# Optimization experiments

Measured on AMD Instinct MI355X. Metric: run time of the kernel, lower is better.

Reference implementation:

```python
import jax, jax.numpy as jnp
import numpy as np

# Dimensions (babyGPT-50m: GPT-2-small-ish)
B, T, V, C, H, L = 2, 1024, 50257, 768, 12, 6
D = C // H
STD = 0.02
EPS = 1e-5


def _normal(k, shape):
    return (jax.random.normal(k, shape, dtype=jnp.float32) * STD)


def setup_inputs() -> dict:
    key = jax.random.key(0)
    ks = jax.random.split(key, 12)
    inp = {
        "idx": jax.random.randint(ks[0], (B, T), 0, V, dtype=jnp.int64 if jax.config.jax_enable_x64 else jnp.int32),
        "tok_emb": _normal(ks[1], (V, C)),
        "pos_emb": _normal(ks[2], (1, T, C)),
        # per-layer params stacked along leading L axis
        "ln1_g": jnp.ones((L, C), jnp.float32),
        "ln1_b": jnp.zeros((L, C), jnp.float32),
        "Wq": _normal(ks[3], (L, C, C)), "bq": jnp.zeros((L, C), jnp.float32),
        "Wk": _normal(ks[4], (L, C, C)), "bk": jnp.zeros((L, C), jnp.float32),
        "Wv": _normal(ks[5], (L, C, C)), "bv": jnp.zeros((L, C), jnp.float32),
        "Wp": _normal(ks[6], (L, C, C)), "bp": jnp.zeros((L, C), jnp.float32),
        "ln2_g": jnp.ones((L, C), jnp.float32),
        "ln2_b": jnp.zeros((L, C), jnp.float32),
        "Wf1": _normal(ks[7], (L, C, 4 * C)), "bf1": jnp.zeros((L, 4 * C), jnp.float32),
        "Wf2": _normal(ks[8], (L, 4 * C, C)), "bf2": jnp.zeros((L, C), jnp.float32),
        "lnf_g": jnp.ones((C,), jnp.float32),
        "lnf_b": jnp.zeros((C,), jnp.float32),
        "head_W": _normal(ks[9], (C, V)),  # head has bias=False
    }
    return inp


def _ln(x, g, b):
    m = jnp.mean(x, axis=-1, keepdims=True)
    v = jnp.var(x, axis=-1, keepdims=True)
    return (x - m) * jax.lax.rsqrt(v + EPS) * g + b


def _gpt_forward(idx, tok_emb, pos_emb, ln1_g, ln1_b, Wq, bq, Wk, bk, Wv, bv,
                 Wp, bp, ln2_g, ln2_b, Wf1, bf1, Wf2, bf2, lnf_g, lnf_b, head_W):
    x = tok_emb[idx] + pos_emb[:, :T]          # [B,T,C]; dropout is identity (eval)
    causal = jnp.tril(jnp.ones((T, T), bool))  # same tril mask as the buffer
    scale = 1.0 / np.sqrt(D).astype(np.float32)

    def block(x, p):
        g1, b1, wq, bq_, wk, bk_, wv, bv_, wp, bp_, g2, b2, w1, b1f, w2, b2f = p
        h = _ln(x, g1, b1)
        q = (h @ wq + bq_).reshape(B, T, H, D)
        k = (h @ wk + bk_).reshape(B, T, H, D)
        v = (h @ wv + bv_).reshape(B, T, H, D)
        att = jnp.einsum('bthd,bshd->bhts', q, k) * scale   # [B,H,T,T]
        att = jnp.where(causal, att, jnp.float32(-10000.0))  # masked_fill value
        att = jax.nn.softmax(att, axis=-1)
        y = jnp.einsum('bhts,bshd->bthd', att, v).reshape(B, T, C)
        x = x + y @ wp + bp_
        h2 = _ln(x, g2, b2)
        ff = jax.nn.gelu(h2 @ w1 + b1f, approximate=False) @ w2 + b2f  # exact GELU, dropout=eval
        return x + ff, None

    layer_params = (ln1_g, ln1_b, Wq, bq, Wk, bk, Wv, bv, Wp, bp,
                    ln2_g, ln2_b, Wf1, bf1, Wf2, bf2)
    x, _ = jax.lax.scan(block, x, layer_params)
    x = _ln(x, lnf_g, lnf_b)
    return x @ head_W  # logits [B,T,V]


def reference(idx, tok_emb, pos_emb, ln1_g, ln1_b, Wq, bq, Wk, bk, Wv, bv,
              Wp, bp, ln2_g, ln2_b, Wf1, bf1, Wf2, bf2, lnf_g, lnf_b, head_W):
    return _gpt_forward(idx, tok_emb, pos_emb, ln1_g, ln1_b, Wq, bq, Wk, bk, Wv, bv,
                        Wp, bp, ln2_g, ln2_b, Wf1, bf1, Wf2, bf2, lnf_g, lnf_b, head_W)
```

## Files before the change

### kernel.cpp

```cpp
#include <hip/hip_runtime.h>
#include <hip/hip_bf16.h>
#include <math.h>

#define Bsz 2
#define Tt 1024
#define Vv 50257
#define Cc 768
#define Hh 12
#define Ll 6
#define NTOK (Bsz*Tt)
#define VPAD 50304

typedef __attribute__((ext_vector_type(8))) short bf16x8;
typedef __attribute__((ext_vector_type(8))) unsigned short u16x8;
typedef __attribute__((ext_vector_type(4))) unsigned short u16x4;
typedef __attribute__((ext_vector_type(4))) float f32x4;
typedef unsigned short u16;

static __device__ __forceinline__ u16 f2bf(float f){
  unsigned u = __float_as_uint(f);
  u += 0x7FFF + ((u >> 16) & 1);
  return (u16)(u >> 16);
}
static __device__ __forceinline__ float bf2f(u16 h){
  return __uint_as_float(((unsigned)h) << 16);
}

#define GL16(g,l) __builtin_amdgcn_global_load_lds( \
    (const __attribute__((address_space(1))) void*)(g), \
    (__attribute__((address_space(3))) void*)(l), 16, 0, 0)
#define WAITVM(n) asm volatile("s_waitcnt vmcnt(%0)" :: "n"(n) : "memory")

__global__ void embed_kernel(const int* __restrict__ idx, const float* __restrict__ tok,
                             const float* __restrict__ pos, float* __restrict__ x){
  const int C4 = Cc/4;
  int i = blockIdx.x * 256 + threadIdx.x;
  if (i >= NTOK*C4) return;
  int tk = i / C4, c4 = i % C4;
  int row = idx[tk];
  int t = tk % Tt;
  float4 a = ((const float4*)tok)[(size_t)row*C4 + c4];
  float4 p = ((const float4*)pos)[(size_t)t*C4 + c4];
  float4 r; r.x=a.x+p.x; r.y=a.y+p.y; r.z=a.z+p.z; r.w=a.w+p.w;
  ((float4*)x)[i] = r;
}

__global__ void ln_kernel(const float* __restrict__ in, const float* __restrict__ g,
                          const float* __restrict__ bt, u16* __restrict__ out){
  int row = blockIdx.x, tid = threadIdx.x;
  const float* r = in + (size_t)row*Cc;
  float v0=r[tid], v1=r[tid+256], v2=r[tid+512];
  float s  = v0+v1+v2;
  float s2 = v0*v0+v1*v1+v2*v2;
  #pragma unroll
  for (int off=32; off; off>>=1){ s += __shfl_xor(s,off); s2 += __shfl_xor(s2,off); }
  __shared__ float red[8];
  int wid = tid >> 6;
  if ((tid & 63) == 0){ red[wid]=s; red[4+wid]=s2; }
  __syncthreads();
  float S  = red[0]+red[1]+red[2]+red[3];
  float S2 = red[4]+red[5]+red[6]+red[7];
  float mean = S * (1.0f/Cc);
  float var  = S2 * (1.0f/Cc) - mean*mean;
  float rstd = rsqrtf(var + 1e-5f);
  u16* o = out + (size_t)row*Cc;
  o[tid]     = f2bf((v0-mean)*rstd*g[tid]     + bt[tid]);
  o[tid+256] = f2bf((v1-mean)*rstd*g[tid+256] + bt[tid+256]);
  o[tid+512] = f2bf((v2-mean)*rstd*g[tid+512] + bt[tid+512]);
}

__global__ void wtrans_kernel(const float* __restrict__ in, u16* __restrict__ out,
                              int K, int N, int Npad, size_t lsi, size_t lso){
  __shared__ float t[64][33];
  const float* inp = in + (size_t)blockIdx.z*lsi;
  u16* op = out + (size_t)blockIdx.z*lso;
  int n0 = blockIdx.x*32, k0 = blockIdx.y*64;
  int tx = threadIdx.x, ty = threadIdx.y;
  #pragma unroll
  for (int i=0;i<8;i++){
    int k = k0+ty+i*8, n = n0+tx;
    t[ty+i*8][tx] = (n < N) ? inp[(size_t)k*N + n] : 0.f;
  }
  __syncthreads();
  #pragma unroll
  for (int i=0;i<2;i++){
    int nl = i*16 + ty*2 + (tx>>4);
    int kl = (tx&15)*4;
    int n = n0 + nl;
    if (n < Npad){
      u16x4 pk;
      pk[0] = f2bf(t[kl+0][nl]); pk[1] = f2bf(t[kl+1][nl]);
      pk[2] = f2bf(t[kl+2][nl]); pk[3] = f2bf(t[kl+3][nl]);
      *(u16x4*)&op[(size_t)n*K + k0 + kl] = pk;
    }
  }
}

__global__ void vtrans_kernel(const u16* __restrict__ qkv, u16* __restrict__ vT){
  __shared__ u16 s[32][33];
  int bh = blockIdx.z; int b = bh/Hh, h = bh - b*Hh;
  int t0 = blockIdx.x*32, d0 = blockIdx.y*32;
  int tx=threadIdx.x, ty=threadIdx.y;
  #pragma unroll
  for (int i=0;i<4;i++)
    s[ty+i*8][tx] = qkv[(size_t)(b*Tt + t0+ty+i*8)*2304 + 1536 + h*64 + d0 + tx];
  __syncthreads();
  #pragma unroll
  for (int i=0;i<4;i++)
    vT[((size_t)bh*64 + d0+ty+i*8)*Tt + t0 + tx] = s[tx][ty+i*8];
}

__global__ void bconcat_kernel(const float* __restrict__ bq, const float* __restrict__ bk,
                               const float* __restrict__ bv, float* __restrict__ o){
  int i = blockIdx.x*256 + threadIdx.x;
  if (i >= Ll*2304) return;
  int l = i/2304, j = i - l*2304;
  o[i] = (j < 768) ? bq[l*768+j] : (j < 1536) ? bk[l*768+j-768] : bv[l*768+j-1536];
}

__global__ __launch_bounds__(256) void flash_kernel(
    const u16* __restrict__ qkv, const u16* __restrict__ vT, u16* __restrict__ y){
  __shared__ u16 Ks[2][64*64];
  __shared__ u16 Vs[2][64*64];
  __shared__ u16 Ps[4][32*64];
  int bx = blockIdx.x;
  int bh = blockIdx.y; int b = bh/Hh, h = bh - b*Hh;
  int q0 = bx*128;
  int tid = threadIdx.x, lane = tid&63, wid = tid>>6;
  const size_t tokbase = (size_t)b*Tt;
  int arow = lane&15, akof = (lane>>4)*8;
  bf16x8 qa[2][2];
  #pragma unroll
  for (int mi=0;mi<2;mi++)
    #pragma unroll
    for (int ks=0;ks<2;ks++)
      qa[mi][ks] = *(const bf16x8*)&qkv[(tokbase + q0 + wid*32 + mi*16 + arow)*2304
                                        + h*64 + ks*32 + akof];
  int srow = lane>>3;
  int sbyte = ((lane&7)*16) ^ (srow<<4);
  const u16* kbase = qkv + tokbase*2304 + 768 + h*64;
  const u16* vbase = vT + (size_t)bh*64*Tt;
  auto STAGEKV = [&](int t, int bb){
    int j0 = t*64;
    #pragma unroll
    for (int c=0;c<2;c++){
      int r = wid*16 + c*8 + srow;
      GL16(kbase + (size_t)(j0 + r)*2304 + (sbyte>>1), &Ks[bb][(wid*16 + c*8)*64]);
      GL16(vbase + (size_t)r*Tt + j0 + (sbyte>>1),     &Vs[bb][(wid*16 + c*8)*64]);
    }
  };
  float m_r[2][4], l_r[2][4];
  f32x4 o_acc[2][4] = {};
  #pragma unroll
  for (int mi=0;mi<2;mi++)
    #pragma unroll
    for (int jj=0;jj<4;jj++){ m_r[mi][jj] = -1e30f; l_r[mi][jj] = 0.f; }

  int njt = 2*bx + 2;
  STAGEKV(0, 0);
  asm volatile("s_waitcnt vmcnt(0)" ::: "memory");
  __builtin_amdgcn_s_barrier();
  for (int t=0; t<njt; t++){
    int cur = t&1;
    if (t+1 < njt) STAGEKV(t+1, cur^1);
    int j0 = t*64;
    f32x4 sacc[2][4] = {};
    #pragma unroll
    for (int ks=0;ks<2;ks++){
      bf16x8 kf[4];
      #pragma unroll
      for (int ni=0;ni<4;ni++){
        int s16 = ni*16 + (lane&15);
        int kb = (ks*64 + (lane>>4)*16) ^ ((s16&7)<<4);
        kf[ni] = *(const bf16x8*)((const char*)&Ks[cur][0] + s16*128 + kb);
      }
      #pragma unroll
      for (int mi=0;mi<2;mi++)
        #pragma unroll
        for (int ni=0;ni<4;ni++)
          sacc[mi][ni] = __builtin_amdgcn_mfma_f32_16x16x32_bf16(qa[mi][ks], kf[ni], sacc[mi][ni], 0,0,0);
    }
    float tmax[2][4];
    #pragma unroll
    for (int mi=0;mi<2;mi++)
      #pragma unroll
      for (int jj=0;jj<4;jj++) tmax[mi][jj] = -1e30f;
    #pragma unroll
    for (int mi=0;mi<2;mi++)
      #pragma unroll
      for (int ni=0;ni<4;ni++)
        #pragma unroll
        for (int jj=0;jj<4;jj++){
          float v = sacc[mi][ni][jj]*0.125f;
          int sg = j0 + ni*16 + (lane&15);
          int tg = q0 + wid*32 + mi*16 + (lane>>4)*4 + jj;
          v = (sg <= tg) ? v : -1e30f;
          sacc[mi][ni][jj] = v;
          tmax[mi][jj] = fmaxf(tmax[mi][jj], v);
        }
    #pragma unroll
    for (int mi=0;mi<2;mi++)
      #pragma unroll
      for (int jj=0;jj<4;jj++){
        float tm = tmax[mi][jj];
        tm = fmaxf(tm, __shfl_xor(tm,1)); tm = fmaxf(tm, __shfl_xor(tm,2));
        tm = fmaxf(tm, __shfl_xor(tm,4)); tm = fmaxf(tm, __shfl_xor(tm,8));
        float mn = fmaxf(m_r[mi][jj], tm);
        float al = __expf(m_r[mi][jj] - mn);
        m_r[mi][jj] = mn;
        l_r[mi][jj] *= al;
        tmax[mi][jj] = al;
      }
    float tsum[2][4] = {};
    #pragma unroll
    for (int mi=0;mi<2;mi++)
      #pragma unroll
      for (int ni=0;ni<4;ni++)
        #pragma unroll
        for (int jj=0;jj<4;jj++){
          float p = __expf(sacc[mi][ni][jj] - m_r[mi][jj]);
          tsum[mi][jj] += p;
          int pr = mi*16 + (lane>>4)*4 + jj;
          int pcb = (2*(ni*16 + (lane&15))) ^ ((pr&7)<<4);
          *(u16*)((char*)&Ps[wid][0] + pr*128 + pcb) = f2bf(p);
        }
    #pragma unroll
    for (int mi=0;mi<2;mi++)
      #pragma unroll
      for (int jj=0;jj<4;jj++){
        float ts = tsum[mi][jj];
        ts += __shfl_xor(ts,1); ts += __shfl_xor(ts,2);
        ts += __shfl_xor(ts,4); ts += __shfl_xor(ts,8);
        l_r[mi][jj] += ts;
        float al = tmax[mi][jj];
        #pragma unroll
        for (int ni2=0;ni2<4;ni2++) o_acc[mi][ni2][jj] *= al;
      }
    #pragma unroll
    for (int ks2=0;ks2<2;ks2++){
      bf16x8 pa[2], vf[4];
      #pragma unroll
      for (int mi=0;mi<2;mi++){
        int prr = mi*16 + (lane&15);
        int pb = (ks2*64 + (lane>>4)*16) ^ ((prr&7)<<4);
        pa[mi] = *(const bf16x8*)((const char*)&Ps[wid][0] + prr*128 + pb);
      }
      #pragma unroll
      for (int ni2=0;ni2<4;ni2++){
        int d16 = ni2*16 + (lane&15);
        int sb = (ks2*64 + (lane>>4)*16) ^ ((d16&7)<<4);
        vf[ni2] = *(const bf16x8*)((const char*)&Vs[cur][0] + d16*128 + sb);
      }
      #pragma unroll
      for (int mi=0;mi<2;mi++)
        #pragma unroll
        for (int ni2=0;ni2<4;ni2++)
          o_acc[mi][ni2] = __builtin_amdgcn_mfma_f32_16x16x32_bf16(pa[mi], vf[ni2], o_acc[mi][ni2], 0,0,0);
    }
    asm volatile("s_waitcnt vmcnt(0) lgkmcnt(0)" ::: "memory");
    __builtin_amdgcn_s_barrier();
  }
  #pragma unroll
  for (int mi=0;mi<2;mi++)
    #pragma unroll
    for (int jj=0;jj<4;jj++){
      float inv = 1.0f / l_r[mi][jj];
      int tok2 = q0 + wid*32 + mi*16 + (lane>>4)*4 + jj;
      size_t rb = (tokbase + tok2)*Cc + h*64;
      #pragma unroll
      for (int ni2=0;ni2<4;ni2++)
        y[rb + ni2*16 + (lane&15)] = f2bf(o_acc[mi][ni2][jj] * inv);
    }
}

template<int BM, int BN, bool BIAS, bool RESID, bool GELU, bool OUTBF, bool ROWSCAN>
__global__ __launch_bounds__(256) void mm_kernel(
    const u16* __restrict__ A, const u16* __restrict__ Bm,
    const float* __restrict__ bias, const float* __restrict__ resid,
    void* __restrict__ out, int N, int K, int lda, int ldb, int ldc)
{
  constexpr int FM   = BM/32;
  constexpr int FN   = BN/32;
  constexpr int CPW  = FN*16;
  constexpr int ESTR = CPW + 4;
  constexpr int ABUF = BM*32;
  constexpr int BBUF = BN*32;
  constexpr int LOADS = (BM+BN)/64;
  constexpr int SMEM_STAGE = 3*(ABUF+BBUF)*2;
  constexpr int SMEM_EPI   = 4*16*ESTR*4;
  constexpr int SMEMB = SMEM_STAGE > SMEM_EPI ? SMEM_STAGE : SMEM_EPI;
  __shared__ __align__(16) char smem[SMEMB];
  u16* As = (u16*)smem;
  u16* Bs = As + 3*ABUF;

  int bx = blockIdx.x, by = blockIdx.y;
  {
    int gx = gridDim.x;
    int nwg = gx * gridDim.y;
    int flat = by*gx + bx;
    int qq = nwg >> 3, rr = nwg & 7;
    int xcd = flat & 7, lid = flat >> 3;
    int swz = (xcd < rr) ? xcd*(qq+1) + lid : rr*(qq+1) + (xcd-rr)*qq + lid;
    bx = swz % gx; by = swz / gx;
  }
  int m0 = bx*BM, n0 = by*BN;
  int tid = threadIdx.x, lane = tid & 63, wid = tid >> 6;
  int wr = wid >> 1, wc = wid & 1;
  int r0 = wr*(BM/2), c0 = wc*(BN/2);
  int lrow = lane & 15, koff = (lane >> 4)*8;
  int sr = lane >> 2, sk = (lane & 3)*8;
  const u16* Ap = A + (size_t)(m0 + wid*(BM/4) + sr)*lda + sk;
  const u16* Bp = Bm + (size_t)(n0 + wid*(BN/4) + sr)*ldb + sk;
  int nt = K/32;
  auto STAGE = [&](int t, int bb){
    int kk = t*32;
    u16* Al = As + bb*ABUF + wid*(ABUF/4);
    GL16(Ap + kk, Al);
    if constexpr (BM==128) GL16(Ap + kk + (size_t)16*lda, Al + 512);
    u16* Bl = Bs + bb*BBUF + wid*(BBUF/4);
    GL16(Bp + kk, Bl);
    if constexpr (BN==128) GL16(Bp + kk + (size_t)16*ldb, Bl + 512);
  };
  f32x4 acc[FM][FN] = {};
  STAGE(0, 0);
  if (nt > 1) STAGE(1, 1);
  WAITVM(LOADS);
  __builtin_amdgcn_s_barrier();
  for (int t = 0; t < nt; t++){
    int bb = t % 3;
    if (t+2 < nt) STAGE(t+2, (t+2)%3);
    const u16* Ab2 = As + bb*ABUF;
    const u16* Bb2 = Bs + bb*BBUF;
    bf16x8 af[FM], bfr[FN];
    #pragma unroll
    for (int m=0;m<FM;m++) af[m] = *(const bf16x8*)&Ab2[(r0 + m*16 + lrow)*32 + koff];
    #pragma unroll
    for (int n=0;n<FN;n++) bfr[n] = *(const bf16x8*)&Bb2[(c0 + n*16 + lrow)*32 + koff];
    #pragma unroll
    for (int m=0;m<FM;m++)
      #pragma unroll
      for (int n=0;n<FN;n++)
        acc[m][n] = __builtin_amdgcn_mfma_f32_16x16x32_bf16(af[m], bfr[n], acc[m][n], 0,0,0);
    if (t+2 < nt) WAITVM(LOADS); else WAITVM(0);
    __builtin_amdgcn_s_barrier();
  }

  float* ebuf = (float*)smem + wid*16*ESTR;
  int er = lane >> 2;
  int ec = (lane & 3) * (CPW/4);
  #pragma unroll
  for (int m=0;m<FM;m++){
    #pragma unroll
    for (int n=0;n<FN;n++)
      #pragma unroll
      for (int j=0;j<4;j++)
        ebuf[((lane>>4)*4+j)*ESTR + n*16 + (lane&15)] = acc[m][n][j];
    __builtin_amdgcn_s_waitcnt(0);
    if constexpr (ROWSCAN){
      #pragma unroll
      for (int rr2=0; rr2<16; rr2++){
        int gr2 = m0 + r0 + m*16 + rr2;
        int gc2 = n0 + c0 + lane;
        float v = ebuf[rr2*ESTR + lane];
        if (gc2 < N) ((float*)out)[(size_t)gr2*ldc + gc2] = v;
      }
    } else {
      int grow = m0 + r0 + m*16 + er;
      int gcol = n0 + c0 + ec;
      size_t rbase = (size_t)grow*ldc;
      if constexpr (OUTBF){
        u16 tmp[CPW/4];
        #pragma unroll
        for (int q=0;q<FN;q++){
          float4 v = *(const float4*)&ebuf[er*ESTR + ec + q*4];
          float f0=v.x, f1=v.y, f2=v.z, f3=v.w;
          if (BIAS){
            float4 b4 = *(const float4*)&bias[gcol + q*4];
            f0+=b4.x; f1+=b4.y; f2+=b4.z; f3+=b4.w;
          }
          if (GELU){
            f0 = 0.5f*f0*(1.f+erff(f0*0.70710678118654752f));
            f1 = 0.5f*f1*(1.f+erff(f1*0.70710678118654752f));
            f2 = 0.5f*f2*(1.f+erff(f2*0.70710678118654752f));
            f3 = 0.5f*f3*(1.f+erff(f3*0.70710678118654752f));
          }
          tmp[q*4+0]=f2bf(f0); tmp[q*4+1]=f2bf(f1);
          tmp[q*4+2]=f2bf(f2); tmp[q*4+3]=f2bf(f3);
        }
        #pragma unroll
        for (int s2=0; s2<CPW/32; s2++)
          *(u16x8*)&((u16*)out)[rbase + gcol + s2*8] = *(const u16x8*)&tmp[s2*8];
      } else {
        #pragma unroll
        for (int q=0;q<FN;q++){
          float4 v = *(const float4*)&ebuf[er*ESTR + ec + q*4];
          float f0=v.x, f1=v.y, f2=v.z, f3=v.w;
          if (BIAS){
            float4 b4 = *(const float4*)&bias[gcol + q*4];
            f0+=b4.x; f1+=b4.y; f2+=b4.z; f3+=b4.w;
          }
          if (GELU){
            f0 = 0.5f*f0*(1.f+erff(f0*0.70710678118654752f));
            f1 = 0.5f*f1*(1.f+erff(f1*0.70710678118654752f));
            f2 = 0.5f*f2*(1.f+erff(f2*0.70710678118654752f));
            f3 = 0.5f*f3*(1.f+erff(f3*0.70710678118654752f));
          }
          if (RESID){
            float4 r4 = *(const float4*)&resid[rbase + gcol + q*4];
            f0+=r4.x; f1+=r4.y; f2+=r4.z; f3+=r4.w;
          }
          float4 o4; o4.x=f0; o4.y=f1; o4.z=f2; o4.w=f3;
          *(float4*)&((float*)out)[rbase + gcol + q*4] = o4;
        }
      }
    }
  }
}

extern "C" void kernel_launch(void* const* d_in, const int* in_sizes, int n_in,
                              void* d_out, int out_size, void* d_ws, size_t ws_size,
                              hipStream_t stream){
  const int*   idx  = (const int*)d_in[0];
  const float* tok  = (const float*)d_in[1];
  const float* pos  = (const float*)d_in[2];
  const float* ln1g = (const float*)d_in[3];
  const float* ln1b = (const float*)d_in[4];
  const float* Wq   = (const float*)d_in[5];
  const float* bq   = (const float*)d_in[6];
  const float* Wk   = (const float*)d_in[7];
  const float* bk   = (const float*)d_in[8];
  const float* Wv   = (const float*)d_in[9];
  const float* bv   = (const float*)d_in[10];
  const float* Wp   = (const float*)d_in[11];
  const float* bp   = (const float*)d_in[12];
  const float* ln2g = (const float*)d_in[13];
  const float* ln2b = (const float*)d_in[14];
  const float* Wf1  = (const float*)d_in[15];
  const float* bf1  = (const float*)d_in[16];
  const float* Wf2  = (const float*)d_in[17];
  const float* bf2  = (const float*)d_in[18];
  const float* lnfg = (const float*)d_in[19];
  const float* lnfb = (const float*)d_in[20];
  const float* headW= (const float*)d_in[21];
  float* outp = (float*)d_out;

  char* w = (char*)d_ws;
  u16* wqkvT = (u16*)w;  w += (size_t)Ll*2304*768*2;
  u16* wpT   = (u16*)w;  w += (size_t)Ll*768*768*2;
  u16* wf1T  = (u16*)w;  w += (size_t)Ll*3072*768*2;
  u16* wf2T  = (u16*)w;  w += (size_t)Ll*768*3072*2;
  u16* headT = (u16*)w;  w += (size_t)VPAD*768*2;
  float* bqkv= (float*)w;w += (size_t)Ll*2304*4;
  float* x   = (float*)w;w += (size_t)NTOK*Cc*4;
  u16* h     = (u16*)w;  w += (size_t)NTOK*Cc*2;
  u16* qkv   = (u16*)w;  w += (size_t)NTOK*2304*2;
  u16* vT    = (u16*)w;  w += (size_t)Bsz*Hh*64*Tt*2;
  u16* y     = (u16*)w;  w += (size_t)NTOK*Cc*2;
  u16* ff    = (u16*)w;  w += (size_t)NTOK*4*Cc*2;

  dim3 tb(32,8);
  wtrans_kernel<<<dim3(24,12,Ll), tb, 0, stream>>>(Wq, wqkvT,          768, 768, 768, (size_t)Cc*Cc, (size_t)2304*768);
  wtrans_kernel<<<dim3(24,12,Ll), tb, 0, stream>>>(Wk, wqkvT+768*768,  768, 768, 768, (size_t)Cc*Cc, (size_t)2304*768);
  wtrans_kernel<<<dim3(24,12,Ll), tb, 0, stream>>>(Wv, wqkvT+1536*768, 768, 768, 768, (size_t)Cc*Cc, (size_t)2304*768);
  wtrans_kernel<<<dim3(24,12,Ll), tb, 0, stream>>>(Wp, wpT,            768, 768, 768, (size_t)Cc*Cc, (size_t)768*768);
  wtrans_kernel<<<dim3(96,12,Ll), tb, 0, stream>>>(Wf1, wf1T,          768, 3072, 3072, (size_t)Cc*4*Cc, (size_t)3072*768);
  wtrans_kernel<<<dim3(24,48,Ll), tb, 0, stream>>>(Wf2, wf2T,          3072, 768, 768, (size_t)4*Cc*Cc, (size_t)768*3072);
  wtrans_kernel<<<dim3(VPAD/32,12,1), tb, 0, stream>>>(headW, headT, 768, Vv, VPAD, 0, 0);
  bconcat_kernel<<<(Ll*2304+255)/256, 256, 0, stream>>>(bq, bk, bv, bqkv);

  embed_kernel<<<NTOK*(Cc/4)/256, 256, 0, stream>>>(idx, tok, pos, x);

  for (int l=0;l<Ll;l++){
    ln_kernel<<<NTOK, 256, 0, stream>>>(x, ln1g+l*Cc, ln1b+l*Cc, h);
    mm_kernel<64,128,true,false,false,true,false><<<dim3(32,18,1), 256, 0, stream>>>(
        h, wqkvT+(size_t)l*2304*768, bqkv+l*2304, nullptr, qkv, 2304, 768, 768, 768, 2304);
    vtrans_kernel<<<dim3(32,2,Bsz*Hh), tb, 0, stream>>>(qkv, vT);
    flash_kernel<<<dim3(Tt/128, Bsz*Hh), 256, 0, stream>>>(qkv, vT, y);
    mm_kernel<64,64,true,true,false,false,false><<<dim3(32,12,1), 256, 0, stream>>>(
        y, wpT+(size_t)l*768*768, bp+l*Cc, x, x, 768, 768, 768, 768, 768);
    ln_kernel<<<NTOK, 256, 0, stream>>>(x, ln2g+l*Cc, ln2b+l*Cc, h);
    mm_kernel<64,128,true,false,true,true,false><<<dim3(32,24,1), 256, 0, stream>>>(
        h, wf1T+(size_t)l*3072*768, bf1+(size_t)l*4*Cc, nullptr, ff, 3072, 768, 768, 768, 3072);
    mm_kernel<64,64,true,true,false,false,false><<<dim3(32,12,1), 256, 0, stream>>>(
        ff, wf2T+(size_t)l*768*3072, bf2+l*Cc, x, x, 768, 3072, 3072, 3072, 768);
  }
  ln_kernel<<<NTOK, 256, 0, stream>>>(x, lnfg, lnfb, h);
  mm_kernel<128,128,false,false,false,false,true><<<dim3(16,VPAD/128,1), 256, 0, stream>>>(
      h, headT, nullptr, nullptr, outp, Vv, 768, 768, 768, Vv);
}
```

Measured before the change: 1.330 ms.

## Shrink flash query tile, double-buffer head GEMM, nontemporal logits stores

The flash attention kernel now processes 64 query rows per block, one 16-row MFMA tile per wave, instead of 128. This doubles the grid and lowers register and LDS use, which should improve occupancy and balance the causal workload. The matmul kernel gains an NBUF template parameter, and the large LM-head GEMM drops from triple to double buffering to cut LDS use per block. Logits are written with nontemporal stores so they do not pollute the cache. In exchange, each K/V tile staged in shared memory is reused by fewer query rows, and the head GEMM keeps less load latency in flight.

```diff
diff --git a/kernel.cpp b/kernel.cpp
--- a/kernel.cpp
+++ b/kernel.cpp
@@ -122,20 +122,18 @@
     const u16* __restrict__ qkv, const u16* __restrict__ vT, u16* __restrict__ y){
   __shared__ u16 Ks[2][64*64];
   __shared__ u16 Vs[2][64*64];
-  __shared__ u16 Ps[4][32*64];
+  __shared__ u16 Ps[4][16*64];
   int bx = blockIdx.x;
   int bh = blockIdx.y; int b = bh/Hh, h = bh - b*Hh;
-  int q0 = bx*128;
+  int q0 = bx*64;
   int tid = threadIdx.x, lane = tid&63, wid = tid>>6;
   const size_t tokbase = (size_t)b*Tt;
   int arow = lane&15, akof = (lane>>4)*8;
-  bf16x8 qa[2][2];
-  #pragma unroll
-  for (int mi=0;mi<2;mi++)
-    #pragma unroll
-    for (int ks=0;ks<2;ks++)
-      qa[mi][ks] = *(const bf16x8*)&qkv[(tokbase + q0 + wid*32 + mi*16 + arow)*2304
-                                        + h*64 + ks*32 + akof];
+  bf16x8 qa[2];
+  #pragma unroll
+  for (int ks=0;ks<2;ks++)
+    qa[ks] = *(const bf16x8*)&qkv[(tokbase + q0 + wid*16 + arow)*2304
+                                  + h*64 + ks*32 + akof];
   int srow = lane>>3;
   int sbyte = ((lane&7)*16) ^ (srow<<4);
   const u16* kbase = qkv + tokbase*2304 + 768 + h*64;
@@ -149,14 +147,12 @@
       GL16(vbase + (size_t)r*Tt + j0 + (sbyte>>1),     &Vs[bb][(wid*16 + c*8)*64]);
     }
   };
-  float m_r[2][4], l_r[2][4];
-  f32x4 o_acc[2][4] = {};
-  #pragma unroll
-  for (int mi=0;mi<2;mi++)
-    #pragma unroll
-    for (int jj=0;jj<4;jj++){ m_r[mi][jj] = -1e30f; l_r[mi][jj] = 0.f; }
-
-  int njt = 2*bx + 2;
+  float m_r[4], l_r[4];
+  f32x4 o_acc[4] = {};
+  #pragma unroll
+  for (int jj=0;jj<4;jj++){ m_r[jj] = -1e30f; l_r[jj] = 0.f; }
+
+  int njt = bx + 1;
   STAGEKV(0, 0);
   asm volatile("s_waitcnt vmcnt(0)" ::: "memory");
   __builtin_amdgcn_s_barrier();
@@ -164,7 +160,7 @@
     int cur = t&1;
     if (t+1 < njt) STAGEKV(t+1, cur^1);
     int j0 = t*64;
-    f32x4 sacc[2][4] = {};
+    f32x4 sacc[4] = {};
     #pragma unroll
     for (int ks=0;ks<2;ks++){
       bf16x8 kf[4];
@@ -175,76 +171,61 @@
         kf[ni] = *(const bf16x8*)((const char*)&Ks[cur][0] + s16*128 + kb);
       }
       #pragma unroll
-      for (int mi=0;mi<2;mi++)
-        #pragma unroll
-        for (int ni=0;ni<4;ni++)
-          sacc[mi][ni] = __builtin_amdgcn_mfma_f32_16x16x32_bf16(qa[mi][ks], kf[ni], sacc[mi][ni], 0,0,0);
-    }
-    float tmax[2][4];
-    #pragma unroll
-    for (int mi=0;mi<2;mi++)
-      #pragma unroll
-      for (int jj=0;jj<4;jj++) tmax[mi][jj] = -1e30f;
-    #pragma unroll
-    for (int mi=0;mi<2;mi++)
-      #pragma unroll
       for (int ni=0;ni<4;ni++)
-        #pragma unroll
-        for (int jj=0;jj<4;jj++){
-          float v = sacc[mi][ni][jj]*0.125f;
-          int sg = j0 + ni*16 + (lane&15);
-          int tg = q0 + wid*32 + mi*16 + (lane>>4)*4 + jj;
-          v = (sg <= tg) ? v : -1e30f;
-          sacc[mi][ni][jj] = v;
-          tmax[mi][jj] = fmaxf(tmax[mi][jj], v);
-        }
-    #pragma unroll
-    for (int mi=0;mi<2;mi++)
+        sacc[ni] = __builtin_amdgcn_mfma_f32_16x16x32_bf16(qa[ks], kf[ni], sacc[ni], 0,0,0);
+    }
+    float tmax[4];
+    #pragma unroll
+    for (int jj=0;jj<4;jj++) tmax[jj] = -1e30f;
+    #pragma unroll
+    for (int ni=0;ni<4;ni++)
       #pragma unroll
       for (int jj=0;jj<4;jj++){
-        float tm = tmax[mi][jj];
-        tm = fmaxf(tm, __shfl_xor(tm,1)); tm = fmaxf(tm, __shfl_xor(tm,2));
-        tm = fmaxf(tm, __shfl_xor(tm,4)); tm = fmaxf(tm, __shfl_xor(tm,8));
-        float mn = fmaxf(m_r[mi][jj], tm);
-        float al = __expf(m_r[mi][jj] - mn);
-        m_r[mi][jj] = mn;
-        l_r[mi][jj] *= al;
-        tmax[mi][jj] = al;
-      }
-    float tsum[2][4] = {};
-    #pragma unroll
-    for (int mi=0;mi<2;mi++)
-      #pragma unroll
-      for (int ni=0;ni<4;ni++)
-        #pragma unroll
-        for (int jj=0;jj<4;jj++){
-          float p = __expf(sacc[mi][ni][jj] - m_r[mi][jj]);
-          tsum[mi][jj] += p;
-          int pr = mi*16 + (lane>>4)*4 + jj;
-          int pcb = (2*(ni*16 + (lane&15))) ^ ((pr&7)<<4);
-          *(u16*)((char*)&Ps[wid][0] + pr*128 + pcb) = f2bf(p);
-        }
-    #pragma unroll
-    for (int mi=0;mi<2;mi++)
+        float v = sacc[ni][jj]*0.125f;
+        int sg = j0 + ni*16 + (lane&15);
+        int tg = q0 + wid*16 + (lane>>4)*4 + jj;
+        v = (sg <= tg) ? v : -1e30f;
+        sacc[ni][jj] = v;
+        tmax[jj] = fmaxf(tmax[jj], v);
+      }
+    #pragma unroll
+    for (int jj=0;jj<4;jj++){
+      float tm = tmax[jj];
+      tm = fmaxf(tm, __shfl_xor(tm,1)); tm = fmaxf(tm, __shfl_xor(tm,2));
+      tm = fmaxf(tm, __shfl_xor(tm,4)); tm = fmaxf(tm, __shfl_xor(tm,8));
+      float mn = fmaxf(m_r[jj], tm);
+      float al = __expf(m_r[jj] - mn);
+      m_r[jj] = mn;
+      l_r[jj] *= al;
+      tmax[jj] = al;
+    }
+    float tsum[4] = {};
+    #pragma unroll
+    for (int ni=0;ni<4;ni++)
       #pragma unroll
       for (int jj=0;jj<4;jj++){
-        float ts = tsum[mi][jj];
-        ts += __shfl_xor(ts,1); ts += __shfl_xor(ts,2);
-        ts += __shfl_xor(ts,4); ts += __shfl_xor(ts,8);
-        l_r[mi][jj] += ts;
-        float al = tmax[mi][jj];
-        #pragma unroll
-        for (int ni2=0;ni2<4;ni2++) o_acc[mi][ni2][jj] *= al;
-      }
+        float p = __expf(sacc[ni][jj] - m_r[jj]);
+        tsum[jj] += p;
+        int pr = (lane>>4)*4 + jj;
+        int pcb = (2*(ni*16 + (lane&15))) ^ ((pr&7)<<4);
+        *(u16*)((char*)&Ps[wid][0] + pr*128 + pcb) = f2bf(p);
+      }
+    #pragma unroll
+    for (int jj=0;jj<4;jj++){
+      float ts = tsum[jj];
+      ts += __shfl_xor(ts,1); ts += __shfl_xor(ts,2);
+      ts += __shfl_xor(ts,4); ts += __shfl_xor(ts,8);
+      l_r[jj] += ts;
+      float al = tmax[jj];
+      #pragma unroll
+      for (int ni2=0;ni2<4;ni2++) o_acc[ni2][jj] *= al;
+    }
     #pragma unroll
     for (int ks2=0;ks2<2;ks2++){
-      bf16x8 pa[2], vf[4];
-      #pragma unroll
-      for (int mi=0;mi<2;mi++){
-        int prr = mi*16 + (lane&15);
-        int pb = (ks2*64 + (lane>>4)*16) ^ ((prr&7)<<4);
-        pa[mi] = *(const bf16x8*)((const char*)&Ps[wid][0] + prr*128 + pb);
-      }
+      bf16x8 pa, vf[4];
+      int prr = lane&15;
+      int pb = (ks2*64 + (lane>>4)*16) ^ ((prr&7)<<4);
+      pa = *(const bf16x8*)((const char*)&Ps[wid][0] + prr*128 + pb);
       #pragma unroll
       for (int ni2=0;ni2<4;ni2++){
         int d16 = ni2*16 + (lane&15);
@@ -252,28 +233,24 @@
         vf[ni2] = *(const bf16x8*)((const char*)&Vs[cur][0] + d16*128 + sb);
       }
       #pragma unroll
-      for (int mi=0;mi<2;mi++)
-        #pragma unroll
-        for (int ni2=0;ni2<4;ni2++)
-          o_acc[mi][ni2] = __builtin_amdgcn_mfma_f32_16x16x32_bf16(pa[mi], vf[ni2], o_acc[mi][ni2], 0,0,0);
+      for (int ni2=0;ni2<4;ni2++)
+        o_acc[ni2] = __builtin_amdgcn_mfma_f32_16x16x32_bf16(pa, vf[ni2], o_acc[ni2], 0,0,0);
     }
     asm volatile("s_waitcnt vmcnt(0) lgkmcnt(0)" ::: "memory");
     __builtin_amdgcn_s_barrier();
   }
   #pragma unroll
-  for (int mi=0;mi<2;mi++)
-    #pragma unroll
-    for (int jj=0;jj<4;jj++){
-      float inv = 1.0f / l_r[mi][jj];
-      int tok2 = q0 + wid*32 + mi*16 + (lane>>4)*4 + jj;
-      size_t rb = (tokbase + tok2)*Cc + h*64;
-      #pragma unroll
-      for (int ni2=0;ni2<4;ni2++)
-        y[rb + ni2*16 + (lane&15)] = f2bf(o_acc[mi][ni2][jj] * inv);
-    }
-}
-
-template<int BM, int BN, bool BIAS, bool RESID, bool GELU, bool OUTBF, bool ROWSCAN>
+  for (int jj=0;jj<4;jj++){
+    float inv = 1.0f / l_r[jj];
+    int tok2 = q0 + wid*16 + (lane>>4)*4 + jj;
+    size_t rb = (tokbase + tok2)*Cc + h*64;
+    #pragma unroll
+    for (int ni2=0;ni2<4;ni2++)
+      y[rb + ni2*16 + (lane&15)] = f2bf(o_acc[ni2][jj] * inv);
+  }
+}
+
+template<int NBUF, int BM, int BN, bool BIAS, bool RESID, bool GELU, bool OUTBF, bool ROWSCAN>
 __global__ __launch_bounds__(256) void mm_kernel(
     const u16* __restrict__ A, const u16* __restrict__ Bm,
     const float* __restrict__ bias, const float* __restrict__ resid,
@@ -286,12 +263,12 @@
   constexpr int ABUF = BM*32;
   constexpr int BBUF = BN*32;
   constexpr int LOADS = (BM+BN)/64;
-  constexpr int SMEM_STAGE = 3*(ABUF+BBUF)*2;
+  constexpr int SMEM_STAGE = NBUF*(ABUF+BBUF)*2;
   constexpr int SMEM_EPI   = 4*16*ESTR*4;
   constexpr int SMEMB = SMEM_STAGE > SMEM_EPI ? SMEM_STAGE : SMEM_EPI;
   __shared__ __align__(16) char smem[SMEMB];
   u16* As = (u16*)smem;
-  u16* Bs = As + 3*ABUF;
+  u16* Bs = As + NBUF*ABUF;
 
   int bx = blockIdx.x, by = blockIdx.y;
   {
@@ -322,13 +299,23 @@
     if constexpr (BN==128) GL16(Bp + kk + (size_t)16*ldb, Bl + 512);
   };
   f32x4 acc[FM][FN] = {};
-  STAGE(0, 0);
-  if (nt > 1) STAGE(1, 1);
-  WAITVM(LOADS);
-  __builtin_amdgcn_s_barrier();
+  if constexpr (NBUF==2){
+    STAGE(0, 0);
+    WAITVM(0);
+    __builtin_amdgcn_s_barrier();
+  } else {
+    STAGE(0, 0);
+    if (nt > 1) STAGE(1, 1);
+    WAITVM(LOADS);
+    __builtin_amdgcn_s_barrier();
+  }
   for (int t = 0; t < nt; t++){
-    int bb = t % 3;
-    if (t+2 < nt) STAGE(t+2, (t+2)%3);
+    int bb = (NBUF==2) ? (t & 1) : (t % 3);
+    if constexpr (NBUF==2){
+      if (t+1 < nt) STAGE(t+1, (t+1)&1);
+    } else {
+      if (t+2 < nt) STAGE(t+2, (t+2)%3);
+    }
     const u16* Ab2 = As + bb*ABUF;
     const u16* Bb2 = Bs + bb*BBUF;
     bf16x8 af[FM], bfr[FN];
@@ -341,7 +328,11 @@
       #pragma unroll
       for (int n=0;n<FN;n++)
         acc[m][n] = __builtin_amdgcn_mfma_f32_16x16x32_bf16(af[m], bfr[n], acc[m][n], 0,0,0);
-    if (t+2 < nt) WAITVM(LOADS); else WAITVM(0);
+    if constexpr (NBUF==2){
+      asm volatile("s_waitcnt vmcnt(0) lgkmcnt(0)" ::: "memory");
+    } else {
+      if (t+2 < nt) WAITVM(LOADS); else WAITVM(0);
+    }
     __builtin_amdgcn_s_barrier();
   }
 
@@ -362,7 +353,8 @@
         int gr2 = m0 + r0 + m*16 + rr2;
         int gc2 = n0 + c0 + lane;
         float v = ebuf[rr2*ESTR + lane];
-        if (gc2 < N) ((float*)out)[(size_t)gr2*ldc + gc2] = v;
+        if (gc2 < N)
+          __builtin_nontemporal_store(v, &((float*)out)[(size_t)gr2*ldc + gc2]);
       }
     } else {
       int grow = m0 + r0 + m*16 + er;
@@ -472,19 +464,19 @@
 
   for (int l=0;l<Ll;l++){
     ln_kernel<<<NTOK, 256, 0, stream>>>(x, ln1g+l*Cc, ln1b+l*Cc, h);
-    mm_kernel<64,128,true,false,false,true,false><<<dim3(32,18,1), 256, 0, stream>>>(
+    mm_kernel<3,64,128,true,false,false,true,false><<<dim3(32,18,1), 256, 0, stream>>>(
         h, wqkvT+(size_t)l*2304*768, bqkv+l*2304, nullptr, qkv, 2304, 768, 768, 768, 2304);
     vtrans_kernel<<<dim3(32,2,Bsz*Hh), tb, 0, stream>>>(qkv, vT);
-    flash_kernel<<<dim3(Tt/128, Bsz*Hh), 256, 0, stream>>>(qkv, vT, y);
-    mm_kernel<64,64,true,true,false,false,false><<<dim3(32,12,1), 256, 0, stream>>>(
+    flash_kernel<<<dim3(Tt/64, Bsz*Hh), 256, 0, stream>>>(qkv, vT, y);
+    mm_kernel<3,64,64,true,true,false,false,false><<<dim3(32,12,1), 256, 0, stream>>>(
         y, wpT+(size_t)l*768*768, bp+l*Cc, x, x, 768, 768, 768, 768, 768);
     ln_kernel<<<NTOK, 256, 0, stream>>>(x, ln2g+l*Cc, ln2b+l*Cc, h);
-    mm_kernel<64,128,true,false,true,true,false><<<dim3(32,24,1), 256, 0, stream>>>(
+    mm_kernel<3,64,128,true,false,true,true,false><<<dim3(32,24,1), 256, 0, stream>>>(
         h, wf1T+(size_t)l*3072*768, bf1+(size_t)l*4*Cc, nullptr, ff, 3072, 768, 768, 768, 3072);
-    mm_kernel<64,64,true,true,false,false,false><<<dim3(32,12,1), 256, 0, stream>>>(
+    mm_kernel<3,64,64,true,true,false,false,false><<<dim3(32,12,1), 256, 0, stream>>>(
         ff, wf2T+(size_t)l*768*3072, bf2+l*Cc, x, x, 768, 3072, 3072, 3072, 768);
   }
   ln_kernel<<<NTOK, 256, 0, stream>>>(x, lnfg, lnfb, h);
-  mm_kernel<128,128,false,false,false,false,true><<<dim3(16,VPAD/128,1), 256, 0, stream>>>(
+  mm_kernel<2,128,128,false,false,false,false,true><<<dim3(16,VPAD/128,1), 256, 0, stream>>>(
       h, headT, nullptr, nullptr, outp, Vv, 768, 768, 768, Vv);
 }
```

Result: faster. 1.249 ms (-6.1%).
